# Optimization experiments

Hardware: AMD Instinct MI355X
Metric: run time of the kernel (lower is better)

Reference implementation:

```python
import jax, jax.numpy as jnp
import numpy as np
from math import pi

TWO_PI = 2.0 * pi

def ringify(x):
    return (x + pi) % TWO_PI - pi

def complex_mean(x, axes):
    dir_x = ringify(jnp.cos(x)).sum(axis=axes)
    dir_y = jnp.sin(x).sum(axis=axes)
    return jnp.arctan2(dir_y, dir_x)

def extract_patches(x, k, s):
    # x: (B, C, H, W) -> (B, Ho, Wo, C, k, k)
    B, C, H, W = x.shape
    Ho = (H - k) // s + 1
    Wo = (W - k) // s + 1
    idx_h = jnp.arange(Ho)[:, None] * s + jnp.arange(k)[None, :]  # (Ho, k)
    idx_w = jnp.arange(Wo)[:, None] * s + jnp.arange(k)[None, :]  # (Wo, k)
    # advanced indexing on dims 2,3 with broadcast shape (Ho, Wo, k, k)
    p = x[:, :, idx_h[:, None, :, None], idx_w[None, :, None, :]]  # (B, C, Ho, Wo, k, k)
    return p.transpose(0, 2, 3, 1, 4, 5)

def ring_conv2d(x, weight, kernel_size, stride):
    # x: (B, C, H, W); weight: (O, C, k, k) -> out: (B, Ho, Wo, O)
    patches = extract_patches(x, kernel_size, stride)            # (B,Ho,Wo,C,k,k)
    w = weight.transpose(1, 2, 3, 0)                              # (C,k,k,O)
    diff = ringify(patches[..., None] - w)                        # (B,Ho,Wo,C,k,k,O)
    return complex_mean(diff, axes=(-4, -3, -2))                  # (B,Ho,Wo,O)

def setup_inputs() -> dict:
    key = jax.random.key(0)
    k1, k2, k3, k4 = jax.random.split(key, 4)
    return {
        "x": jax.random.normal(k1, (4096, 1, 28, 28), dtype=jnp.float32),
        "conv1_weight": jax.random.normal(k2, (4, 1, 2, 2), dtype=jnp.float32),
        "conv2_weight": jax.random.normal(k3, (8, 4, 4, 4), dtype=jnp.float32),
        "ff_weight": jax.random.normal(k4, (288, 10), dtype=jnp.float32),
    }

def reference(x, conv1_weight, conv2_weight, ff_weight):
    h = ringify(x).reshape(-1, 1, 28, 28)
    h = ring_conv2d(h, conv1_weight, kernel_size=2, stride=2)     # (B,14,14,4)
    h = h.transpose(0, 3, 1, 2)                                   # (B,4,14,14)
    h = ring_conv2d(h, conv2_weight, kernel_size=4, stride=2)     # (B,6,6,8)
    h = h.reshape(h.shape[0], -1)                                 # (B,288)
    h = complex_mean(ringify(h[:, :, None] - ff_weight), axes=(-2,))  # (B,10)
    return jnp.sin(h)
```

## Files before the change

kernel.cpp:

```cpp
#include <hip/hip_runtime.h>

#define WT_W1 0
#define WT_W2 16
#define WT_FF 528

typedef _Float16 h2 __attribute__((ext_vector_type(2)));

__device__ __forceinline__ float fdot2(unsigned a, unsigned b, float c) {
    return __builtin_amdgcn_fdot2(__builtin_bit_cast(h2, a),
                                  __builtin_bit_cast(h2, b), c, false);
}
__device__ __forceinline__ unsigned packh2(float x, float y) {
    h2 h; h.x = (_Float16)x; h.y = (_Float16)y;
    return __builtin_bit_cast(unsigned, h);
}

__global__ void ringnn_setup(const float* __restrict__ w1,
                             const float* __restrict__ w2,
                             const float* __restrict__ ffw,
                             uint2* __restrict__ wt) {
    int t = blockIdx.x * blockDim.x + threadIdx.x;
    if (t >= 3408) return;
    float a;
    if (t < 16)        a = w1[t];
    else if (t < 528)  a = w2[t - 16];
    else               a = ffw[t - 528];
    float s, c;
    __sincosf(a, &s, &c);
    uint2 v;
    v.x = packh2(c, s);
    v.y = packh2(-s, c);
    wt[t] = v;
}

__global__ __launch_bounds__(256) void ringnn_main(
    const float* __restrict__ x,
    const uint2* __restrict__ wt,
    float* __restrict__ out)
{
    __shared__ unsigned cs1[4][784];
    __shared__ unsigned cs2[4][288];

    const int t    = threadIdx.x;
    const int wv   = t >> 6;
    const int lane = t & 63;
    const int b    = blockIdx.x * 4 + wv;
    const float* xb = x + b * 784;

    for (int pos = lane; pos < 196; pos += 64) {
        const int i = pos / 14;
        const int j = pos - i * 14;
        const float* px = xb + (2 * i) * 28 + 2 * j;
        float2 p0 = *(const float2*)(px);
        float2 p1 = *(const float2*)(px + 28);
        float s0, c0, s1, c1, s2, c2, s3, c3;
        __sincosf(p0.x, &s0, &c0);
        __sincosf(p0.y, &s1, &c1);
        __sincosf(p1.x, &s2, &c2);
        __sincosf(p1.y, &s3, &c3);
        unsigned v0 = packh2(c0, s0), v1 = packh2(c1, s1);
        unsigned v2 = packh2(c2, s2), v3 = packh2(c3, s3);
        #pragma unroll
        for (int o = 0; o < 4; ++o) {
            uint2 wa = wt[WT_W1 + o * 4 + 0], wb = wt[WT_W1 + o * 4 + 1];
            uint2 wc = wt[WT_W1 + o * 4 + 2], wd = wt[WT_W1 + o * 4 + 3];
            float X = 0.f, Y = 0.f;
            X = fdot2(v0, wa.x, X); Y = fdot2(v0, wa.y, Y);
            X = fdot2(v1, wb.x, X); Y = fdot2(v1, wb.y, Y);
            X = fdot2(v2, wc.x, X); Y = fdot2(v2, wc.y, Y);
            X = fdot2(v3, wd.x, X); Y = fdot2(v3, wd.y, Y);
            float rinv = rsqrtf(fmaxf(fmaf(X, X, Y * Y), 1e-30f));
            cs1[wv][o * 196 + pos] = packh2(X * rinv, Y * rinv);
        }
    }

    if (lane < 36) {
        const int i = lane / 6;
        const int j = lane - i * 6;
        const unsigned* cb = &cs1[wv][(2 * i) * 14 + 2 * j];
        float X0=0.f,X1=0.f,X2=0.f,X3=0.f,X4=0.f,X5=0.f,X6=0.f,X7=0.f;
        float Y0=0.f,Y1=0.f,Y2=0.f,Y3=0.f,Y4=0.f,Y5=0.f,Y6=0.f,Y7=0.f;
        #pragma unroll
        for (int c = 0; c < 4; ++c) {
            uint2 a[4][2];
            #pragma unroll
            for (int dy = 0; dy < 4; ++dy) {
                const unsigned* r = cb + c * 196 + dy * 14;
                a[dy][0] = *(const uint2*)(r);
                a[dy][1] = *(const uint2*)(r + 2);
            }
            #pragma unroll
            for (int o = 0; o < 8; ++o) {
                float Xa = 0.f, Ya = 0.f;
                const uint2* wp = wt + WT_W2 + o * 64 + c * 16;
                #pragma unroll
                for (int dy = 0; dy < 4; ++dy) {
                    uint2 w0 = wp[dy * 4 + 0], w1_ = wp[dy * 4 + 1];
                    uint2 w2_ = wp[dy * 4 + 2], w3_ = wp[dy * 4 + 3];
                    Xa = fdot2(a[dy][0].x, w0.x, Xa); Ya = fdot2(a[dy][0].x, w0.y, Ya);
                    Xa = fdot2(a[dy][0].y, w1_.x, Xa); Ya = fdot2(a[dy][0].y, w1_.y, Ya);
                    Xa = fdot2(a[dy][1].x, w2_.x, Xa); Ya = fdot2(a[dy][1].x, w2_.y, Ya);
                    Xa = fdot2(a[dy][1].y, w3_.x, Xa); Ya = fdot2(a[dy][1].y, w3_.y, Ya);
                }
                switch (o) {
                    case 0: X0 += Xa; Y0 += Ya; break;
                    case 1: X1 += Xa; Y1 += Ya; break;
                    case 2: X2 += Xa; Y2 += Ya; break;
                    case 3: X3 += Xa; Y3 += Ya; break;
                    case 4: X4 += Xa; Y4 += Ya; break;
                    case 5: X5 += Xa; Y5 += Ya; break;
                    case 6: X6 += Xa; Y6 += Ya; break;
                    case 7: X7 += Xa; Y7 += Ya; break;
                }
            }
        }
        unsigned rr[8];
        {
            float Xs[8] = {X0,X1,X2,X3,X4,X5,X6,X7};
            float Ys[8] = {Y0,Y1,Y2,Y3,Y4,Y5,Y6,Y7};
            #pragma unroll
            for (int o = 0; o < 8; ++o) {
                float rv = rsqrtf(fmaxf(fmaf(Xs[o], Xs[o], Ys[o] * Ys[o]), 1e-30f));
                rr[o] = packh2(Xs[o] * rv, Ys[o] * rv);
            }
        }
        uint2* dst = (uint2*)&cs2[wv][lane * 8];
        dst[0] = make_uint2(rr[0], rr[1]);
        dst[1] = make_uint2(rr[2], rr[3]);
        dst[2] = make_uint2(rr[4], rr[5]);
        dst[3] = make_uint2(rr[6], rr[7]);
    }

    {
        float X = 0.f, Y = 0.f;
        const int n = lane / 6;
        const int g = lane - n * 6;
        if (n < 10) {
            #pragma unroll 6
            for (int k = 0; k < 48; ++k) {
                const int f = g + 6 * k;
                unsigned v = cs2[wv][f];
                uint2 wvv = wt[WT_FF + f * 10 + n];
                X = fdot2(v, wvv.x, X);
                Y = fdot2(v, wvv.y, Y);
            }
        }
        float pX = X + __shfl_down(X, 3);
        float pY = Y + __shfl_down(Y, 3);
        float sX = pX + __shfl_down(pX, 1) + __shfl_down(pX, 2);
        float sY = pY + __shfl_down(pY, 1) + __shfl_down(pY, 2);
        if (g == 0 && n < 10) {
            float rinv = rsqrtf(fmaxf(fmaf(sX, sX, sY * sY), 1e-30f));
            out[b * 10 + n] = sY * rinv;
        }
    }
}

extern "C" void kernel_launch(void* const* d_in, const int* in_sizes, int n_in,
                              void* d_out, int out_size, void* d_ws, size_t ws_size,
                              hipStream_t stream) {
    const float* x   = (const float*)d_in[0];
    const float* w1  = (const float*)d_in[1];
    const float* w2  = (const float*)d_in[2];
    const float* ffw = (const float*)d_in[3];
    uint2* wt = (uint2*)d_ws;
    float* o  = (float*)d_out;

    ringnn_setup<<<14, 256, 0, stream>>>(w1, w2, ffw, wt);
    ringnn_main<<<1024, 256, 0, stream>>>(x, wt, o);
}
```

Baseline: 85.82 us.

## Compute conv2 with MFMA 16x16x32 f16 across two images per block

Moves the second ring convolution from per-lane fdot2 loops onto MFMA matrix instructions. Conv2 weights are pre-packed by the setup kernel into a B-fragment layout, and each block now processes two images with two wavefronts that share the 72 output positions as 16-row tiles. Adjacent accumulator columns hold X and Y and are paired with lane shuffles. The block shrinks to 128 threads with twice as many blocks. This adds block-wide barriers and tile clamping for the unused tail rows.

```diff
diff --git a/kernel.cpp b/kernel.cpp
--- a/kernel.cpp
+++ b/kernel.cpp
@@ -3,8 +3,11 @@
 #define WT_W1 0
 #define WT_W2 16
 #define WT_FF 528
+#define WT_B2_BYTES (3408 * 8)
 
-typedef _Float16 h2 __attribute__((ext_vector_type(2)));
+typedef _Float16 h2  __attribute__((ext_vector_type(2)));
+typedef _Float16 v8h __attribute__((ext_vector_type(8)));
+typedef float    f4  __attribute__((ext_vector_type(4)));
 
 __device__ __forceinline__ float fdot2(unsigned a, unsigned b, float c) {
     return __builtin_amdgcn_fdot2(__builtin_bit_cast(h2, a),
@@ -20,32 +23,49 @@
                              const float* __restrict__ ffw,
                              uint2* __restrict__ wt) {
     int t = blockIdx.x * blockDim.x + threadIdx.x;
-    if (t >= 3408) return;
-    float a;
-    if (t < 16)        a = w1[t];
-    else if (t < 528)  a = w2[t - 16];
-    else               a = ffw[t - 528];
-    float s, c;
-    __sincosf(a, &s, &c);
-    uint2 v;
-    v.x = packh2(c, s);
-    v.y = packh2(-s, c);
-    wt[t] = v;
+    if (t < 3408) {
+        float a;
+        if (t < 16)        a = w1[t];
+        else if (t < 528)  a = w2[t - 16];
+        else               a = ffw[t - 528];
+        float s, c;
+        __sincosf(a, &s, &c);
+        uint2 v;
+        v.x = packh2(c, s);
+        v.y = packh2(-s, c);
+        wt[t] = v;
+    } else if (t < 3408 + 256) {
+        const int e  = t - 3408;
+        const int nn = e & 15;
+        const int dy = (e >> 4) & 3;
+        const int c  = e >> 6;
+        const int o  = nn >> 1;
+        unsigned d[4];
+        #pragma unroll
+        for (int dx = 0; dx < 4; ++dx) {
+            float a = w2[o * 64 + c * 16 + dy * 4 + dx];
+            float s, cc;
+            __sincosf(a, &s, &cc);
+            d[dx] = (nn & 1) ? packh2(-s, cc) : packh2(cc, s);
+        }
+        uint4* Bt = (uint4*)((char*)wt + WT_B2_BYTES);
+        Bt[e] = make_uint4(d[0], d[1], d[2], d[3]);
+    }
 }
 
-__global__ __launch_bounds__(256) void ringnn_main(
+__global__ __launch_bounds__(128) void ringnn_main(
     const float* __restrict__ x,
     const uint2* __restrict__ wt,
     float* __restrict__ out)
 {
-    __shared__ unsigned cs1[4][784];
-    __shared__ unsigned cs2[4][288];
+    __shared__ unsigned cs1[2][784];
+    __shared__ unsigned cs2[2][288];
 
     const int t    = threadIdx.x;
     const int wv   = t >> 6;
     const int lane = t & 63;
-    const int b    = blockIdx.x * 4 + wv;
-    const float* xb = x + b * 784;
+    const int b0   = blockIdx.x * 2;
+    const float* xb = x + (b0 + wv) * 784;
 
     for (int pos = lane; pos < 196; pos += 64) {
         const int i = pos / 14;
@@ -74,73 +94,69 @@
         }
     }
 
-    if (lane < 36) {
-        const int i = lane / 6;
-        const int j = lane - i * 6;
-        const unsigned* cb = &cs1[wv][(2 * i) * 14 + 2 * j];
-        float X0=0.f,X1=0.f,X2=0.f,X3=0.f,X4=0.f,X5=0.f,X6=0.f,X7=0.f;
-        float Y0=0.f,Y1=0.f,Y2=0.f,Y3=0.f,Y4=0.f,Y5=0.f,Y6=0.f,Y7=0.f;
+    const int n    = lane & 15;
+    const int quad = lane >> 4;
+    const uint4* Bt = (const uint4*)((const char*)wt + WT_B2_BYTES);
+    uint4 bf0 = Bt[lane];
+    uint4 bf1 = Bt[64 + lane];
+    uint4 bf2 = Bt[128 + lane];
+    uint4 bf3 = Bt[192 + lane];
+
+    __syncthreads();
+
+    const unsigned* c1 = &cs1[0][0];
+    for (int tile = wv; tile < 5; tile += 2) {
+        const int p  = tile * 16 + n;
+        const int pc = (p < 72) ? p : 71;
+        const int im = (pc >= 36) ? 1 : 0;
+        const int ps = pc - im * 36;
+        const int i  = ps / 6;
+        const int j  = ps - i * 6;
+        const unsigned base = (unsigned)(im * 784 + (2 * i + quad) * 14 + 2 * j);
+        f4 acc = {0.f, 0.f, 0.f, 0.f};
         #pragma unroll
         for (int c = 0; c < 4; ++c) {
-            uint2 a[4][2];
+            uint2 lo = *(const uint2*)(c1 + base + c * 196);
+            uint2 hi = *(const uint2*)(c1 + base + c * 196 + 2);
+            uint4 a4 = make_uint4(lo.x, lo.y, hi.x, hi.y);
+            v8h av = __builtin_bit_cast(v8h, a4);
+            v8h bv = __builtin_bit_cast(v8h, (c == 0) ? bf0 : (c == 1) ? bf1
+                                              : (c == 2) ? bf2 : bf3);
+            acc = __builtin_amdgcn_mfma_f32_16x16x32_f16(av, bv, acc, 0, 0, 0);
+        }
+        float pr0 = __shfl_xor(acc[0], 1);
+        float pr1 = __shfl_xor(acc[1], 1);
+        float pr2 = __shfl_xor(acc[2], 1);
+        float pr3 = __shfl_xor(acc[3], 1);
+        if (!(n & 1)) {
+            const int o = n >> 1;
+            float Xs[4] = {acc[0], acc[1], acc[2], acc[3]};
+            float Ys[4] = {pr0, pr1, pr2, pr3};
             #pragma unroll
-            for (int dy = 0; dy < 4; ++dy) {
-                const unsigned* r = cb + c * 196 + dy * 14;
-                a[dy][0] = *(const uint2*)(r);
-                a[dy][1] = *(const uint2*)(r + 2);
-            }
-            #pragma unroll
-            for (int o = 0; o < 8; ++o) {
-                float Xa = 0.f, Ya = 0.f;
-                const uint2* wp = wt + WT_W2 + o * 64 + c * 16;
-                #pragma unroll
-                for (int dy = 0; dy < 4; ++dy) {
-                    uint2 w0 = wp[dy * 4 + 0], w1_ = wp[dy * 4 + 1];
-                    uint2 w2_ = wp[dy * 4 + 2], w3_ = wp[dy * 4 + 3];
-                    Xa = fdot2(a[dy][0].x, w0.x, Xa); Ya = fdot2(a[dy][0].x, w0.y, Ya);
-                    Xa = fdot2(a[dy][0].y, w1_.x, Xa); Ya = fdot2(a[dy][0].y, w1_.y, Ya);
-                    Xa = fdot2(a[dy][1].x, w2_.x, Xa); Ya = fdot2(a[dy][1].x, w2_.y, Ya);
-                    Xa = fdot2(a[dy][1].y, w3_.x, Xa); Ya = fdot2(a[dy][1].y, w3_.y, Ya);
-                }
-                switch (o) {
-                    case 0: X0 += Xa; Y0 += Ya; break;
-                    case 1: X1 += Xa; Y1 += Ya; break;
-                    case 2: X2 += Xa; Y2 += Ya; break;
-                    case 3: X3 += Xa; Y3 += Ya; break;
-                    case 4: X4 += Xa; Y4 += Ya; break;
-                    case 5: X5 += Xa; Y5 += Ya; break;
-                    case 6: X6 += Xa; Y6 += Ya; break;
-                    case 7: X7 += Xa; Y7 += Ya; break;
+            for (int r = 0; r < 4; ++r) {
+                const int p2 = tile * 16 + quad * 4 + r;
+                if (p2 < 72) {
+                    const int im2 = (p2 >= 36) ? 1 : 0;
+                    const int ps2 = p2 - im2 * 36;
+                    float X = Xs[r], Y = Ys[r];
+                    float rinv = rsqrtf(fmaxf(fmaf(X, X, Y * Y), 1e-30f));
+                    cs2[im2][ps2 * 8 + o] = packh2(X * rinv, Y * rinv);
                 }
             }
         }
-        unsigned rr[8];
-        {
-            float Xs[8] = {X0,X1,X2,X3,X4,X5,X6,X7};
-            float Ys[8] = {Y0,Y1,Y2,Y3,Y4,Y5,Y6,Y7};
-            #pragma unroll
-            for (int o = 0; o < 8; ++o) {
-                float rv = rsqrtf(fmaxf(fmaf(Xs[o], Xs[o], Ys[o] * Ys[o]), 1e-30f));
-                rr[o] = packh2(Xs[o] * rv, Ys[o] * rv);
-            }
-        }
-        uint2* dst = (uint2*)&cs2[wv][lane * 8];
-        dst[0] = make_uint2(rr[0], rr[1]);
-        dst[1] = make_uint2(rr[2], rr[3]);
-        dst[2] = make_uint2(rr[4], rr[5]);
-        dst[3] = make_uint2(rr[6], rr[7]);
     }
+    __syncthreads();
 
     {
         float X = 0.f, Y = 0.f;
-        const int n = lane / 6;
-        const int g = lane - n * 6;
-        if (n < 10) {
+        const int n3 = lane / 6;
+        const int g  = lane - n3 * 6;
+        if (n3 < 10) {
             #pragma unroll 6
             for (int k = 0; k < 48; ++k) {
                 const int f = g + 6 * k;
                 unsigned v = cs2[wv][f];
-                uint2 wvv = wt[WT_FF + f * 10 + n];
+                uint2 wvv = wt[WT_FF + f * 10 + n3];
                 X = fdot2(v, wvv.x, X);
                 Y = fdot2(v, wvv.y, Y);
             }
@@ -149,9 +165,9 @@
         float pY = Y + __shfl_down(Y, 3);
         float sX = pX + __shfl_down(pX, 1) + __shfl_down(pX, 2);
         float sY = pY + __shfl_down(pY, 1) + __shfl_down(pY, 2);
-        if (g == 0 && n < 10) {
+        if (g == 0 && n3 < 10) {
             float rinv = rsqrtf(fmaxf(fmaf(sX, sX, sY * sY), 1e-30f));
-            out[b * 10 + n] = sY * rinv;
+            out[(b0 + wv) * 10 + n3] = sY * rinv;
         }
     }
 }
@@ -166,6 +182,6 @@
     uint2* wt = (uint2*)d_ws;
     float* o  = (float*)d_out;
 
-    ringnn_setup<<<14, 256, 0, stream>>>(w1, w2, ffw, wt);
-    ringnn_main<<<1024, 256, 0, stream>>>(x, wt, o);
+    ringnn_setup<<<15, 256, 0, stream>>>(w1, w2, ffw, wt);
+    ringnn_main<<<2048, 128, 0, stream>>>(x, wt, o);
 }
```

New measurement: 76.97 us. 10.3% less time.
